# Performance work log

Measured on AMD Instinct MI355X. Metric: run time of the kernel, lower is better.

Reference implementation:

```python
import jax, jax.numpy as jnp
import numpy as np
from jax.ops import segment_sum

N_NODES = 100000
N_EDGES = 1600000
N_GRAPHS = 128


def setup_inputs() -> dict:
    key = jax.random.key(0)
    ks = jax.random.split(key, 16)
    x = jax.random.normal(ks[0], (N_NODES, 128), dtype=jnp.float32)
    edge_index = jax.random.randint(ks[1], (2, N_EDGES), 0, N_NODES, dtype=jnp.int64)
    batch = jnp.sort(jax.random.randint(ks[2], (N_NODES,), 0, N_GRAPHS, dtype=jnp.int64))
    def glorot(k, fan_in, fan_out):
        lim = (6.0 / (fan_in + fan_out)) ** 0.5
        return jax.random.uniform(k, (fan_in, fan_out), jnp.float32, -lim, lim)
    return {
        "x": x, "edge_index": edge_index, "batch": batch,
        "W1": glorot(ks[3], 128, 64), "b1": jnp.zeros((64,), jnp.float32),
        "W2": glorot(ks[4], 64, 64),  "b2": jnp.zeros((64,), jnp.float32),
        "W3": glorot(ks[5], 64, 64),  "b3": jnp.zeros((64,), jnp.float32),
        "W4": glorot(ks[6], 64, 64),  "b4": jnp.zeros((64,), jnp.float32),
        "Wl": glorot(ks[7], 64, 1),   "bl": jnp.zeros((1,), jnp.float32),
    }


def _gcn_layer(x, row, col, norm, W, b):
    # x: [N, Cin] -> [N, Cout]; gather source feats, scale, scatter-add at target
    h = x @ W                                 # dense transform first (GCNConv order)
    msg = norm[:, None] * h[row]              # [E, Cout]
    out = segment_sum(msg, col, num_segments=N_NODES)
    return out + b


def reference(x, edge_index, batch, W1, b1, W2, b2, W3, b3, W4, b4, Wl, bl):
    row, col = edge_index[0], edge_index[1]
    # symmetric degree normalization based on in-degree of col (PyG degree(col))
    deg = segment_sum(jnp.ones((N_EDGES,), x.dtype), col, num_segments=N_NODES)
    dinv = jnp.where(deg > 0, deg ** -0.5, jnp.zeros_like(deg))
    norm = dinv[row] * dinv[col]              # [E]

    h = _gcn_layer(x, row, col, norm, W1, b1)
    h = _gcn_layer(h, row, col, norm, W2, b2)
    h = _gcn_layer(h, row, col, norm, W3, b3)
    h = _gcn_layer(h, row, col, norm, W4, b4)  # [N, 64]

    # to_dense_batch + mean(dim=1): padded zeros count, so divide by max graph size
    sums = segment_sum(h, batch, num_segments=N_GRAPHS)          # [B, 64]
    counts = segment_sum(jnp.ones((N_NODES,), h.dtype), batch, num_segments=N_GRAPHS)
    n_max = jnp.max(counts)
    pooled = sums / n_max                                        # [B, 64]
    return pooled @ Wl + bl                                      # [B, 1]
```

## Files before the change

kernel.cpp:

```cpp
#include <hip/hip_runtime.h>
#include <hip/hip_bf16.h>
#include <hip/hip_fp16.h>

#define N_NODES 100000
#define N_EDGES 1600000
#define N_GRAPHS 128

#define BSH 9
#define BNODES 512
#define NB 196
#define CAP 12288
#define BLK 512
#define EPB (N_EDGES / BLK)
#define RECMAX 10240

#define SPLIT 4

typedef __attribute__((ext_vector_type(8))) _Float16 v8h;
typedef __attribute__((ext_vector_type(4))) float v4f;


__global__ __launch_bounds__(256) void k_hist(const int* __restrict__ col,
                                              int* __restrict__ hist_t) {
    __shared__ int h[NB];
    const int t = threadIdx.x, b = blockIdx.x;
    for (int i = t; i < NB; i += 256) h[i] = 0;
    __syncthreads();
    const int e0 = b * EPB;
    for (int i = t; i < EPB; i += 256) atomicAdd(&h[col[e0 + i] >> BSH], 1);
    __syncthreads();
    for (int i = t; i < NB; i += 256) hist_t[i * BLK + b] = h[i];
}

__global__ __launch_bounds__(512) void k_cursors(const int* __restrict__ hist_t,
                                                 int* __restrict__ cursors,
                                                 int* __restrict__ bcnt) {
    __shared__ int s[BLK];
    const int t = threadIdx.x, bin = blockIdx.x;
    const int v = hist_t[bin * BLK + t];
    s[t] = v; __syncthreads();
    for (int off = 1; off < BLK; off <<= 1) {
        int a = (t >= off) ? s[t - off] : 0;
        __syncthreads(); s[t] += a; __syncthreads();
    }
    cursors[bin * BLK + t] = bin * CAP + s[t] - v;
    if (t == BLK - 1) bcnt[bin] = s[t];
}

__global__ __launch_bounds__(256) void k_mid(const int* __restrict__ row,
                                             const int* __restrict__ col,
                                             const int* __restrict__ cursors,
                                             int* __restrict__ bedges) {
    __shared__ int cur[NB];
    const int t = threadIdx.x, b = blockIdx.x;
    for (int i = t; i < NB; i += 256) cur[i] = cursors[i * BLK + b];
    __syncthreads();
    const int e0 = b * EPB;
    for (int i = t; i < EPB; i += 256) {
        const int c = col[e0 + i];
        const int r = row[e0 + i];
        const int pos = atomicAdd(&cur[c >> BSH], 1);
        bedges[pos] = r | ((c & (BNODES - 1)) << 17);
    }
}

__global__ __launch_bounds__(512) void k_build(const int* __restrict__ bedges,
                                               const int* __restrict__ bcnt,
                                               int* __restrict__ csr,
                                               int* __restrict__ offs,
                                               int* __restrict__ deg_c,
                                               float* __restrict__ dinv) {
    __shared__ int rec[RECMAX];
    __shared__ int deg[BNODES];
    __shared__ int offx[BNODES];
    __shared__ int cur[BNODES];
    const int t = threadIdx.x, bin = blockIdx.x;
    const int base = bin * CAP;
    const int cnt = bcnt[bin];
    const int vb = bin << BSH;
    const int nn = min(BNODES, N_NODES - vb);
    for (int i = t; i < cnt; i += 512) rec[i] = bedges[base + i];
    deg[t] = 0;
    __syncthreads();
    for (int i = t; i < cnt; i += 512) atomicAdd(&deg[(rec[i] >> 17) & (BNODES - 1)], 1);
    __syncthreads();
    const int d = (t < nn) ? deg[t] : 0;
    const int pd = (d + 7) & ~7;
    offx[t] = pd; __syncthreads();
    for (int off = 1; off < BNODES; off <<= 1) {
        int a = (t >= off) ? offx[t - off] : 0;
        __syncthreads(); offx[t] += a; __syncthreads();
    }
    const int myoff = offx[t] - pd;
    cur[t] = myoff;
    if (t < nn) {
        offs[vb + t] = base + myoff;
        deg_c[vb + t] = d;
        dinv[vb + t] = (d > 0) ? rsqrtf((float)d) : 0.0f;
        for (int j = d; j < pd; j++) csr[base + myoff + j] = N_NODES;
    }
    __syncthreads();
    for (int i = t; i < cnt; i += 512) {
        const int r = rec[i];
        const int pos = atomicAdd(&cur[(r >> 17) & (BNODES - 1)], 1);
        csr[base + pos] = r & 0x1FFFF;
    }
}


template <int CIN, typename TIN>
__global__ __launch_bounds__(256) void k_gemm(const TIN* __restrict__ X,
                                              const float* __restrict__ W,
                                              const float* __restrict__ dinv,
                                              __half* __restrict__ H16) {
    constexpr int SA = 72;
    constexpr int SB = 72;
    __shared__ __align__(16) _Float16 sA[128 * SA];
    __shared__ __align__(16) _Float16 sBh[64 * SB];
    __shared__ __align__(16) _Float16 sBl[64 * SB];
    const int t = threadIdx.x;
    const int w = t >> 6, lane = t & 63;
    const int quad = lane >> 4, l16 = lane & 15;
    const int nb = blockIdx.x * 128;

    v4f acc[2][4] = {};

    for (int k0 = 0; k0 < CIN; k0 += 64) {
        if (k0) __syncthreads();
        for (int i = t; i < 64 * 16; i += 256) {
            const int k = i >> 4, c4 = (i & 15) * 4;
            const float4 wv = *reinterpret_cast<const float4*>(W + (size_t)(k0 + k) * 64 + c4);
            const float wf[4] = {wv.x, wv.y, wv.z, wv.w};
            #pragma unroll
            for (int j = 0; j < 4; j++) {
                const _Float16 hi = (_Float16)wf[j];
                sBh[(c4 + j) * SB + k] = hi;
                sBl[(c4 + j) * SB + k] = (_Float16)(wf[j] - (float)hi);
            }
        }
        if constexpr (sizeof(TIN) == 4) {
            for (int i = t; i < 128 * 16; i += 256) {
                const int node = i >> 4, k4 = (i & 15) * 4;
                const int gn = nb + node;
                float4 v = make_float4(0.f, 0.f, 0.f, 0.f);
                if (gn < N_NODES)
                    v = *reinterpret_cast<const float4*>((const float*)X + (size_t)gn * CIN + k0 + k4);
                _Float16* d = &sA[node * SA + k4];
                d[0] = (_Float16)v.x; d[1] = (_Float16)v.y;
                d[2] = (_Float16)v.z; d[3] = (_Float16)v.w;
            }
        } else {
            for (int i = t; i < 128 * 8; i += 256) {
                const int node = i >> 3, k8 = (i & 7) * 8;
                const int gn = nb + node;
                int4 v = make_int4(0, 0, 0, 0);
                if (gn < N_NODES)
                    v = *reinterpret_cast<const int4*>((const __half*)X + (size_t)gn * CIN + k0 + k8);
                *reinterpret_cast<int4*>(&sA[node * SA + k8]) = v;
            }
        }
        __syncthreads();

        #pragma unroll
        for (int kt = 0; kt < 2; kt++) {
            const int kb = kt * 32 + quad * 8;
            v8h afr[2], bh[4], bl[4];
            #pragma unroll
            for (int mt = 0; mt < 2; mt++)
                afr[mt] = *reinterpret_cast<const v8h*>(&sA[(w * 32 + mt * 16 + l16) * SA + kb]);
            #pragma unroll
            for (int nt = 0; nt < 4; nt++) {
                bh[nt] = *reinterpret_cast<const v8h*>(&sBh[(nt * 16 + l16) * SB + kb]);
                bl[nt] = *reinterpret_cast<const v8h*>(&sBl[(nt * 16 + l16) * SB + kb]);
            }
            #pragma unroll
            for (int mt = 0; mt < 2; mt++)
                #pragma unroll
                for (int nt = 0; nt < 4; nt++) {
                    acc[mt][nt] = __builtin_amdgcn_mfma_f32_16x16x32_f16(afr[mt], bh[nt], acc[mt][nt], 0, 0, 0);
                    acc[mt][nt] = __builtin_amdgcn_mfma_f32_16x16x32_f16(afr[mt], bl[nt], acc[mt][nt], 0, 0, 0);
                }
        }
    }

    #pragma unroll
    for (int mt = 0; mt < 2; mt++) {
        #pragma unroll
        for (int reg = 0; reg < 4; reg++) {
            const int node = nb + w * 32 + mt * 16 + quad * 4 + reg;
            if (node < N_NODES) {
                const float dv = dinv[node];
                #pragma unroll
                for (int nt = 0; nt < 4; nt++)
                    H16[(size_t)node * 64 + nt * 16 + l16] =
                        __float2half(acc[mt][nt][reg] * dv);
            }
        }
    }
}


template <typename TOUT>
__global__ __launch_bounds__(256) void k_prop(const __half* __restrict__ Hin,
                                              const int* __restrict__ csr,
                                              const int* __restrict__ offs,
                                              const int* __restrict__ deg_c,
                                              const float* __restrict__ dinv,
                                              const float* __restrict__ bias,
                                              TOUT* __restrict__ Hout) {
    const int wave = threadIdx.x >> 6, lane = threadIdx.x & 63;
    const int quad = lane >> 4;
    const int l = lane & 15;
    const int v = blockIdx.x * 16 + wave * 4 + quad;
    const int start = offs[v];
    const int cp = (deg_c[v] + 7) & ~7;
    const int* ep = csr + start;
    const __half* hb = Hin + l * 4;
    float a0 = 0.f, a1 = 0.f, a2 = 0.f, a3 = 0.f;
    for (int j = 0; j < cp; j += 8) {
        const int4 q0 = *reinterpret_cast<const int4*>(ep + j);
        const int4 q1 = *reinterpret_cast<const int4*>(ep + j + 4);
        const int2 r0 = *reinterpret_cast<const int2*>(hb + (size_t)q0.x * 64);
        const int2 r1 = *reinterpret_cast<const int2*>(hb + (size_t)q0.y * 64);
        const int2 r2 = *reinterpret_cast<const int2*>(hb + (size_t)q0.z * 64);
        const int2 r3 = *reinterpret_cast<const int2*>(hb + (size_t)q0.w * 64);
        const int2 r4 = *reinterpret_cast<const int2*>(hb + (size_t)q1.x * 64);
        const int2 r5 = *reinterpret_cast<const int2*>(hb + (size_t)q1.y * 64);
        const int2 r6 = *reinterpret_cast<const int2*>(hb + (size_t)q1.z * 64);
        const int2 r7 = *reinterpret_cast<const int2*>(hb + (size_t)q1.w * 64);
        #define ACC(r) { \
            const float2 u = __half22float2(*reinterpret_cast<const __half2*>(&r.x)); \
            const float2 w = __half22float2(*reinterpret_cast<const __half2*>(&r.y)); \
            a0 += u.x; a1 += u.y; a2 += w.x; a3 += w.y; }
        ACC(r0) ACC(r1) ACC(r2) ACC(r3) ACC(r4) ACC(r5) ACC(r6) ACC(r7)
        #undef ACC
    }
    const float dv = dinv[v];
    const float4 bs = *reinterpret_cast<const float4*>(bias + l * 4);
    const float o0 = dv * a0 + bs.x, o1 = dv * a1 + bs.y;
    const float o2 = dv * a2 + bs.z, o3 = dv * a3 + bs.w;
    if constexpr (sizeof(TOUT) == 2) {
        __half2 h[2];
        h[0] = __floats2half2_rn(o0, o1);
        h[1] = __floats2half2_rn(o2, o3);
        *reinterpret_cast<int2*>((__half*)Hout + (size_t)v * 64 + l * 4) =
            *reinterpret_cast<const int2*>(h);
    } else {
        float4 o; o.x = o0; o.y = o1; o.z = o2; o.w = o3;
        *reinterpret_cast<float4*>((float*)Hout + (size_t)v * 64 + l * 4) = o;
    }
}


__global__ __launch_bounds__(256) void k_pool(const float* __restrict__ H,
                                              const int* __restrict__ batch,
                                              float* __restrict__ partial) {
    const int g = blockIdx.x >> 2;
    const int s = blockIdx.x & (SPLIT - 1);
    int lo = 0, hi = N_NODES;
    while (lo < hi) { int m = (lo + hi) >> 1; if (batch[m] < g) lo = m + 1; else hi = m; }
    const int a = lo;
    lo = 0; hi = N_NODES;
    while (lo < hi) { int m = (lo + hi) >> 1; if (batch[m] < g + 1) lo = m + 1; else hi = m; }
    const int b = lo;

    const int wave = threadIdx.x >> 6, lane = threadIdx.x & 63;
    const int lane16 = s * 4 + wave;
    float ac0 = 0.f, ac1 = 0.f, ac2 = 0.f, ac3 = 0.f;
    int v = a + lane16;
    for (; v + 48 < b; v += 64) {
        ac0 += H[(size_t)v * 64 + lane];
        ac1 += H[(size_t)(v + 16) * 64 + lane];
        ac2 += H[(size_t)(v + 32) * 64 + lane];
        ac3 += H[(size_t)(v + 48) * 64 + lane];
    }
    for (; v < b; v += 16) ac0 += H[(size_t)v * 64 + lane];
    const float acc = (ac0 + ac1) + (ac2 + ac3);

    __shared__ float red[4][64];
    red[wave][lane] = acc;
    __syncthreads();
    if (wave == 0) {
        const float r = (red[0][lane] + red[1][lane]) + (red[2][lane] + red[3][lane]);
        partial[((size_t)s * N_GRAPHS + g) * 64 + lane] = r;
    }
}

__global__ void k_final(const float* __restrict__ partial, const int* __restrict__ batch,
                        const float* __restrict__ Wl, const float* __restrict__ bl,
                        float* __restrict__ out) {
    __shared__ int scnt[128];
    int t = threadIdx.x;
    int lo = 0, hi = N_NODES;
    while (lo < hi) { int mid = (lo + hi) >> 1; if (batch[mid] < t) lo = mid + 1; else hi = mid; }
    int a = lo;
    lo = 0; hi = N_NODES;
    while (lo < hi) { int mid = (lo + hi) >> 1; if (batch[mid] < t + 1) lo = mid + 1; else hi = mid; }
    scnt[t] = lo - a;
    __syncthreads();
    for (int off = 64; off > 0; off >>= 1) {
        if (t < off) scnt[t] = max(scnt[t], scnt[t + off]);
        __syncthreads();
    }
    const float nmax = (float)scnt[0];
    float s = 0.f;
    for (int c = 0; c < 64; c++) {
        float g = 0.f;
        #pragma unroll
        for (int p = 0; p < SPLIT; p++)
            g += partial[((size_t)p * N_GRAPHS + t) * 64 + c];
        s += g * Wl[c];
    }
    out[t] = s / nmax + bl[0];
}


extern "C" void kernel_launch(void* const* d_in, const int* in_sizes, int n_in,
                              void* d_out, int out_size, void* d_ws, size_t ws_size,
                              hipStream_t stream) {
    const float* x    = (const float*)d_in[0];
    const int*   ei   = (const int*)d_in[1];
    const int*   batch= (const int*)d_in[2];
    const float* W1 = (const float*)d_in[3];  const float* b1 = (const float*)d_in[4];
    const float* W2 = (const float*)d_in[5];  const float* b2 = (const float*)d_in[6];
    const float* W3 = (const float*)d_in[7];  const float* b3 = (const float*)d_in[8];
    const float* W4 = (const float*)d_in[9];  const float* b4 = (const float*)d_in[10];
    const float* Wl = (const float*)d_in[11]; const float* bl = (const float*)d_in[12];
    float* out = (float*)d_out;

    const int* row = ei;
    const int* col = ei + N_EDGES;

    char* ws = (char*)d_ws;
    size_t off = 0;
    auto alloc = [&](size_t bytes) {
        void* p = ws + off;
        off = (off + bytes + 255) & ~(size_t)255;
        return p;
    };
    int*    hist_t  = (int*)alloc((size_t)NB * BLK * 4);
    int*    cursors = (int*)alloc((size_t)NB * BLK * 4);
    int*    bcnt    = (int*)alloc(NB * 4);
    int*    bedges  = (int*)alloc((size_t)NB * CAP * 4);
    int*    csr     = bedges;
    int*    offs    = (int*)alloc(N_NODES * 4);
    int*    deg_c   = (int*)alloc(N_NODES * 4);
    float*  dinv    = (float*)alloc(N_NODES * 4);
    __half* h16     = (__half*)alloc((size_t)(N_NODES + 1) * 64 * 2);
    __half* h_c     = (__half*)alloc((size_t)N_NODES * 64 * 2);
    float*  h_b     = (float*)alloc((size_t)N_NODES * 64 * 4);
    float*  partial = (float*)alloc((size_t)SPLIT * N_GRAPHS * 64 * 4);

    hipMemsetAsync(h16 + (size_t)N_NODES * 64, 0, 64 * 2, stream);

    k_hist<<<BLK, 256, 0, stream>>>(col, hist_t);
    k_cursors<<<NB, 512, 0, stream>>>(hist_t, cursors, bcnt);
    k_mid<<<BLK, 256, 0, stream>>>(row, col, cursors, bedges);
    k_build<<<NB, 512, 0, stream>>>(bedges, bcnt, csr, offs, deg_c, dinv);

    const int GB = (N_NODES + 127) / 128;
    const int PB = N_NODES / 16;

    k_gemm<128, float><<<GB, 256, 0, stream>>>(x, W1, dinv, h16);
    k_prop<__half><<<PB, 256, 0, stream>>>(h16, csr, offs, deg_c, dinv, b1, h_c);
    k_gemm<64, __half><<<GB, 256, 0, stream>>>(h_c, W2, dinv, h16);
    k_prop<__half><<<PB, 256, 0, stream>>>(h16, csr, offs, deg_c, dinv, b2, h_c);
    k_gemm<64, __half><<<GB, 256, 0, stream>>>(h_c, W3, dinv, h16);
    k_prop<__half><<<PB, 256, 0, stream>>>(h16, csr, offs, deg_c, dinv, b3, h_c);
    k_gemm<64, __half><<<GB, 256, 0, stream>>>(h_c, W4, dinv, h16);
    k_prop<float><<<PB, 256, 0, stream>>>(h16, csr, offs, deg_c, dinv, b4, h_b);

    k_pool<<<N_GRAPHS * SPLIT, 256, 0, stream>>>(h_b, batch, partial);
    k_final<<<1, 128, 0, stream>>>(partial, batch, Wl, bl, out);
}
```

Baseline: 362.3 us.

## Slice node features into four 16-channel planes for cache-local gather propagation

Stores the 64-channel hidden features as four planes of 16 channels each. Propagation runs one grid dimension per plane, so each plane (about 3.2 MB in fp16) can stay resident in cache while the edge gathers run. Within a quad, lanes now split the edges four ways and combine partial sums with shuffles, and CSR padding grows to 16 with a larger bin capacity. GEMM loads, GEMM stores and pooling are updated to the sliced layout. The cost is reading the CSR index list four times and adding shuffle reductions.

```diff
diff --git a/kernel.cpp b/kernel.cpp
--- a/kernel.cpp
+++ b/kernel.cpp
@@ -9,15 +9,25 @@
 #define BSH 9
 #define BNODES 512
 #define NB 196
-#define CAP 12288
+#define CAP 18432
 #define BLK 512
 #define EPB (N_EDGES / BLK)
 #define RECMAX 10240
 
 #define SPLIT 4
 
+#define NSLICE 4
+#define SLS (N_NODES + 8)
+
 typedef __attribute__((ext_vector_type(8))) _Float16 v8h;
 typedef __attribute__((ext_vector_type(4))) float v4f;
+typedef __attribute__((ext_vector_type(4))) int vi4;
+typedef __attribute__((ext_vector_type(2))) int vi2;
+typedef __attribute__((ext_vector_type(4))) float vf4;
+
+__device__ __forceinline__ float2 h2f(int bits) {
+    return __half22float2(__builtin_bit_cast(__half2, bits));
+}
 
 
 __global__ __launch_bounds__(256) void k_hist(const int* __restrict__ col,
@@ -85,7 +95,7 @@
     for (int i = t; i < cnt; i += 512) atomicAdd(&deg[(rec[i] >> 17) & (BNODES - 1)], 1);
     __syncthreads();
     const int d = (t < nn) ? deg[t] : 0;
-    const int pd = (d + 7) & ~7;
+    const int pd = (d + 15) & ~15;
     offx[t] = pd; __syncthreads();
     for (int off = 1; off < BNODES; off <<= 1) {
         int a = (t >= off) ? offx[t - off] : 0;
@@ -151,12 +161,15 @@
             }
         } else {
             for (int i = t; i < 128 * 8; i += 256) {
-                const int node = i >> 3, k8 = (i & 7) * 8;
+                const int off8 = (i & 1) * 8;
+                const int node = (i >> 1) & 127;
+                const int sl = i >> 8;
                 const int gn = nb + node;
                 int4 v = make_int4(0, 0, 0, 0);
                 if (gn < N_NODES)
-                    v = *reinterpret_cast<const int4*>((const __half*)X + (size_t)gn * CIN + k0 + k8);
-                *reinterpret_cast<int4*>(&sA[node * SA + k8]) = v;
+                    v = *reinterpret_cast<const int4*>(
+                        (const __half*)X + ((size_t)sl * N_NODES + gn) * 16 + off8);
+                *reinterpret_cast<int4*>(&sA[node * SA + sl * 16 + off8]) = v;
             }
         }
         __syncthreads();
@@ -192,7 +205,7 @@
                 const float dv = dinv[node];
                 #pragma unroll
                 for (int nt = 0; nt < 4; nt++)
-                    H16[(size_t)node * 64 + nt * 16 + l16] =
+                    H16[((size_t)nt * SLS + node) * 16 + l16] =
                         __float2half(acc[mt][nt][reg] * dv);
             }
         }
@@ -210,44 +223,48 @@
                                               TOUT* __restrict__ Hout) {
     const int wave = threadIdx.x >> 6, lane = threadIdx.x & 63;
     const int quad = lane >> 4;
-    const int l = lane & 15;
+    const int es = (lane >> 2) & 3;
+    const int cg = lane & 3;
+    const int s = blockIdx.y;
     const int v = blockIdx.x * 16 + wave * 4 + quad;
     const int start = offs[v];
-    const int cp = (deg_c[v] + 7) & ~7;
-    const int* ep = csr + start;
-    const __half* hb = Hin + l * 4;
+    const int cp = (deg_c[v] + 15) & ~15;
+    const int* ep = csr + start + es * 4;
+    const __half* hb = Hin + (size_t)s * SLS * 16 + cg * 4;
     float a0 = 0.f, a1 = 0.f, a2 = 0.f, a3 = 0.f;
-    for (int j = 0; j < cp; j += 8) {
-        const int4 q0 = *reinterpret_cast<const int4*>(ep + j);
-        const int4 q1 = *reinterpret_cast<const int4*>(ep + j + 4);
-        const int2 r0 = *reinterpret_cast<const int2*>(hb + (size_t)q0.x * 64);
-        const int2 r1 = *reinterpret_cast<const int2*>(hb + (size_t)q0.y * 64);
-        const int2 r2 = *reinterpret_cast<const int2*>(hb + (size_t)q0.z * 64);
-        const int2 r3 = *reinterpret_cast<const int2*>(hb + (size_t)q0.w * 64);
-        const int2 r4 = *reinterpret_cast<const int2*>(hb + (size_t)q1.x * 64);
-        const int2 r5 = *reinterpret_cast<const int2*>(hb + (size_t)q1.y * 64);
-        const int2 r6 = *reinterpret_cast<const int2*>(hb + (size_t)q1.z * 64);
-        const int2 r7 = *reinterpret_cast<const int2*>(hb + (size_t)q1.w * 64);
+    for (int j = 0; j < cp; j += 16) {
+        const vi4 e = __builtin_nontemporal_load(reinterpret_cast<const vi4*>(ep + j));
+        const vi2 r0 = *reinterpret_cast<const vi2*>(hb + (size_t)e.x * 16);
+        const vi2 r1 = *reinterpret_cast<const vi2*>(hb + (size_t)e.y * 16);
+        const vi2 r2 = *reinterpret_cast<const vi2*>(hb + (size_t)e.z * 16);
+        const vi2 r3 = *reinterpret_cast<const vi2*>(hb + (size_t)e.w * 16);
         #define ACC(r) { \
-            const float2 u = __half22float2(*reinterpret_cast<const __half2*>(&r.x)); \
-            const float2 w = __half22float2(*reinterpret_cast<const __half2*>(&r.y)); \
+            const float2 u = h2f(r.x); \
+            const float2 w = h2f(r.y); \
             a0 += u.x; a1 += u.y; a2 += w.x; a3 += w.y; }
-        ACC(r0) ACC(r1) ACC(r2) ACC(r3) ACC(r4) ACC(r5) ACC(r6) ACC(r7)
+        ACC(r0) ACC(r1) ACC(r2) ACC(r3)
         #undef ACC
     }
-    const float dv = dinv[v];
-    const float4 bs = *reinterpret_cast<const float4*>(bias + l * 4);
-    const float o0 = dv * a0 + bs.x, o1 = dv * a1 + bs.y;
-    const float o2 = dv * a2 + bs.z, o3 = dv * a3 + bs.w;
-    if constexpr (sizeof(TOUT) == 2) {
-        __half2 h[2];
-        h[0] = __floats2half2_rn(o0, o1);
-        h[1] = __floats2half2_rn(o2, o3);
-        *reinterpret_cast<int2*>((__half*)Hout + (size_t)v * 64 + l * 4) =
-            *reinterpret_cast<const int2*>(h);
-    } else {
-        float4 o; o.x = o0; o.y = o1; o.z = o2; o.w = o3;
-        *reinterpret_cast<float4*>((float*)Hout + (size_t)v * 64 + l * 4) = o;
+    a0 += __shfl_xor(a0, 4); a1 += __shfl_xor(a1, 4);
+    a2 += __shfl_xor(a2, 4); a3 += __shfl_xor(a3, 4);
+    a0 += __shfl_xor(a0, 8); a1 += __shfl_xor(a1, 8);
+    a2 += __shfl_xor(a2, 8); a3 += __shfl_xor(a3, 8);
+    if (es == 0) {
+        const float dv = dinv[v];
+        const float4 bs = *reinterpret_cast<const float4*>(bias + s * 16 + cg * 4);
+        const float o0 = dv * a0 + bs.x, o1 = dv * a1 + bs.y;
+        const float o2 = dv * a2 + bs.z, o3 = dv * a3 + bs.w;
+        if constexpr (sizeof(TOUT) == 2) {
+            vi2 pk;
+            pk.x = __builtin_bit_cast(int, __floats2half2_rn(o0, o1));
+            pk.y = __builtin_bit_cast(int, __floats2half2_rn(o2, o3));
+            __builtin_nontemporal_store(pk,
+                reinterpret_cast<vi2*>((__half*)Hout + ((size_t)s * N_NODES + v) * 16 + cg * 4));
+        } else {
+            vf4 o; o.x = o0; o.y = o1; o.z = o2; o.w = o3;
+            __builtin_nontemporal_store(o,
+                reinterpret_cast<vf4*>((float*)Hout + ((size_t)s * N_NODES + v) * 16 + cg * 4));
+        }
     }
 }
 
@@ -266,15 +283,16 @@
 
     const int wave = threadIdx.x >> 6, lane = threadIdx.x & 63;
     const int lane16 = s * 4 + wave;
+    const size_t sbase = (size_t)(lane >> 4) * ((size_t)N_NODES * 16) + (lane & 15);
     float ac0 = 0.f, ac1 = 0.f, ac2 = 0.f, ac3 = 0.f;
     int v = a + lane16;
     for (; v + 48 < b; v += 64) {
-        ac0 += H[(size_t)v * 64 + lane];
-        ac1 += H[(size_t)(v + 16) * 64 + lane];
-        ac2 += H[(size_t)(v + 32) * 64 + lane];
-        ac3 += H[(size_t)(v + 48) * 64 + lane];
-    }
-    for (; v < b; v += 16) ac0 += H[(size_t)v * 64 + lane];
+        ac0 += H[sbase + (size_t)v * 16];
+        ac1 += H[sbase + (size_t)(v + 16) * 16];
+        ac2 += H[sbase + (size_t)(v + 32) * 16];
+        ac3 += H[sbase + (size_t)(v + 48) * 16];
+    }
+    for (; v < b; v += 16) ac0 += H[sbase + (size_t)v * 16];
     const float acc = (ac0 + ac1) + (ac2 + ac3);
 
     __shared__ float red[4][64];
@@ -346,12 +364,13 @@
     int*    offs    = (int*)alloc(N_NODES * 4);
     int*    deg_c   = (int*)alloc(N_NODES * 4);
     float*  dinv    = (float*)alloc(N_NODES * 4);
-    __half* h16     = (__half*)alloc((size_t)(N_NODES + 1) * 64 * 2);
-    __half* h_c     = (__half*)alloc((size_t)N_NODES * 64 * 2);
-    float*  h_b     = (float*)alloc((size_t)N_NODES * 64 * 4);
+    __half* h16     = (__half*)alloc((size_t)NSLICE * SLS * 16 * 2);
+    __half* h_c     = (__half*)alloc((size_t)NSLICE * N_NODES * 16 * 2);
+    float*  h_b     = (float*)alloc((size_t)NSLICE * N_NODES * 16 * 4);
     float*  partial = (float*)alloc((size_t)SPLIT * N_GRAPHS * 64 * 4);
 
-    hipMemsetAsync(h16 + (size_t)N_NODES * 64, 0, 64 * 2, stream);
+    for (int s = 0; s < NSLICE; ++s)
+        (void)hipMemsetAsync(h16 + ((size_t)s * SLS + N_NODES) * 16, 0, 16 * 2, stream);
 
     k_hist<<<BLK, 256, 0, stream>>>(col, hist_t);
     k_cursors<<<NB, 512, 0, stream>>>(hist_t, cursors, bcnt);
@@ -359,16 +378,16 @@
     k_build<<<NB, 512, 0, stream>>>(bedges, bcnt, csr, offs, deg_c, dinv);
 
     const int GB = (N_NODES + 127) / 128;
-    const int PB = N_NODES / 16;
+    const dim3 gprop(N_NODES / 16, NSLICE);
 
     k_gemm<128, float><<<GB, 256, 0, stream>>>(x, W1, dinv, h16);
-    k_prop<__half><<<PB, 256, 0, stream>>>(h16, csr, offs, deg_c, dinv, b1, h_c);
+    k_prop<__half><<<gprop, 256, 0, stream>>>(h16, csr, offs, deg_c, dinv, b1, h_c);
     k_gemm<64, __half><<<GB, 256, 0, stream>>>(h_c, W2, dinv, h16);
-    k_prop<__half><<<PB, 256, 0, stream>>>(h16, csr, offs, deg_c, dinv, b2, h_c);
+    k_prop<__half><<<gprop, 256, 0, stream>>>(h16, csr, offs, deg_c, dinv, b2, h_c);
     k_gemm<64, __half><<<GB, 256, 0, stream>>>(h_c, W3, dinv, h16);
-    k_prop<__half><<<PB, 256, 0, stream>>>(h16, csr, offs, deg_c, dinv, b3, h_c);
+    k_prop<__half><<<gprop, 256, 0, stream>>>(h16, csr, offs, deg_c, dinv, b3, h_c);
     k_gemm<64, __half><<<GB, 256, 0, stream>>>(h_c, W4, dinv, h16);
-    k_prop<float><<<PB, 256, 0, stream>>>(h16, csr, offs, deg_c, dinv, b4, h_b);
+    k_prop<float><<<gprop, 256, 0, stream>>>(h16, csr, offs, deg_c, dinv, b4, h_b);
 
     k_pool<<<N_GRAPHS * SPLIT, 256, 0, stream>>>(h_b, batch, partial);
     k_final<<<1, 128, 0, stream>>>(partial, batch, Wl, bl, out);
```

After: 503.9 us. 1.39x slower.

## Fuse propagation with next-layer GEMM and use nontemporal CSR loads

Applied to the files above, without the earlier changes.

Merges each intermediate propagation (gather-sum over CSR neighbors) with the following layer's dense transform into one kernel. The aggregated 128-node tile is written straight to LDS as fp16 and fed to MFMA, so the h_c round trip and three kernel launches go away. It also adds nontemporal loads for CSR indices and a nontemporal store for the final fp32 output. The cost is fewer blocks (782 vs 6250) doing latency-bound gathers with large LDS per block, which may lower occupancy and latency hiding.

```diff
diff --git a/kernel.cpp b/kernel.cpp
--- a/kernel.cpp
+++ b/kernel.cpp
@@ -18,6 +18,13 @@
 
 typedef __attribute__((ext_vector_type(8))) _Float16 v8h;
 typedef __attribute__((ext_vector_type(4))) float v4f;
+typedef __attribute__((ext_vector_type(4))) int vi4;
+typedef __attribute__((ext_vector_type(2))) int vi2;
+typedef __attribute__((ext_vector_type(4))) float vf4;
+
+__device__ __forceinline__ float2 h2f(int bits) {
+    return __half22float2(__builtin_bit_cast(__half2, bits));
+}
 
 
 __global__ __launch_bounds__(256) void k_hist(const int* __restrict__ col,
@@ -108,8 +115,8 @@
 }
 
 
-template <int CIN, typename TIN>
-__global__ __launch_bounds__(256) void k_gemm(const TIN* __restrict__ X,
+template <int CIN>
+__global__ __launch_bounds__(256) void k_gemm(const float* __restrict__ X,
                                               const float* __restrict__ W,
                                               const float* __restrict__ dinv,
                                               __half* __restrict__ H16) {
@@ -138,26 +145,15 @@
                 sBl[(c4 + j) * SB + k] = (_Float16)(wf[j] - (float)hi);
             }
         }
-        if constexpr (sizeof(TIN) == 4) {
-            for (int i = t; i < 128 * 16; i += 256) {
-                const int node = i >> 4, k4 = (i & 15) * 4;
-                const int gn = nb + node;
-                float4 v = make_float4(0.f, 0.f, 0.f, 0.f);
-                if (gn < N_NODES)
-                    v = *reinterpret_cast<const float4*>((const float*)X + (size_t)gn * CIN + k0 + k4);
-                _Float16* d = &sA[node * SA + k4];
-                d[0] = (_Float16)v.x; d[1] = (_Float16)v.y;
-                d[2] = (_Float16)v.z; d[3] = (_Float16)v.w;
-            }
-        } else {
-            for (int i = t; i < 128 * 8; i += 256) {
-                const int node = i >> 3, k8 = (i & 7) * 8;
-                const int gn = nb + node;
-                int4 v = make_int4(0, 0, 0, 0);
-                if (gn < N_NODES)
-                    v = *reinterpret_cast<const int4*>((const __half*)X + (size_t)gn * CIN + k0 + k8);
-                *reinterpret_cast<int4*>(&sA[node * SA + k8]) = v;
-            }
+        for (int i = t; i < 128 * 16; i += 256) {
+            const int node = i >> 4, k4 = (i & 15) * 4;
+            const int gn = nb + node;
+            float4 v = make_float4(0.f, 0.f, 0.f, 0.f);
+            if (gn < N_NODES)
+                v = *reinterpret_cast<const float4*>(X + (size_t)gn * CIN + k0 + k4);
+            _Float16* d = &sA[node * SA + k4];
+            d[0] = (_Float16)v.x; d[1] = (_Float16)v.y;
+            d[2] = (_Float16)v.z; d[3] = (_Float16)v.w;
         }
         __syncthreads();
 
@@ -200,14 +196,13 @@
 }
 
 
-template <typename TOUT>
-__global__ __launch_bounds__(256) void k_prop(const __half* __restrict__ Hin,
-                                              const int* __restrict__ csr,
-                                              const int* __restrict__ offs,
-                                              const int* __restrict__ deg_c,
-                                              const float* __restrict__ dinv,
-                                              const float* __restrict__ bias,
-                                              TOUT* __restrict__ Hout) {
+__global__ __launch_bounds__(256) void k_prop_f(const __half* __restrict__ Hin,
+                                                const int* __restrict__ csr,
+                                                const int* __restrict__ offs,
+                                                const int* __restrict__ deg_c,
+                                                const float* __restrict__ dinv,
+                                                const float* __restrict__ bias,
+                                                float* __restrict__ Hout) {
     const int wave = threadIdx.x >> 6, lane = threadIdx.x & 63;
     const int quad = lane >> 4;
     const int l = lane & 15;
@@ -218,36 +213,136 @@
     const __half* hb = Hin + l * 4;
     float a0 = 0.f, a1 = 0.f, a2 = 0.f, a3 = 0.f;
     for (int j = 0; j < cp; j += 8) {
-        const int4 q0 = *reinterpret_cast<const int4*>(ep + j);
-        const int4 q1 = *reinterpret_cast<const int4*>(ep + j + 4);
-        const int2 r0 = *reinterpret_cast<const int2*>(hb + (size_t)q0.x * 64);
-        const int2 r1 = *reinterpret_cast<const int2*>(hb + (size_t)q0.y * 64);
-        const int2 r2 = *reinterpret_cast<const int2*>(hb + (size_t)q0.z * 64);
-        const int2 r3 = *reinterpret_cast<const int2*>(hb + (size_t)q0.w * 64);
-        const int2 r4 = *reinterpret_cast<const int2*>(hb + (size_t)q1.x * 64);
-        const int2 r5 = *reinterpret_cast<const int2*>(hb + (size_t)q1.y * 64);
-        const int2 r6 = *reinterpret_cast<const int2*>(hb + (size_t)q1.z * 64);
-        const int2 r7 = *reinterpret_cast<const int2*>(hb + (size_t)q1.w * 64);
+        const vi4 q0 = __builtin_nontemporal_load(reinterpret_cast<const vi4*>(ep + j));
+        const vi4 q1 = __builtin_nontemporal_load(reinterpret_cast<const vi4*>(ep + j + 4));
+        const vi2 r0 = *reinterpret_cast<const vi2*>(hb + (size_t)q0.x * 64);
+        const vi2 r1 = *reinterpret_cast<const vi2*>(hb + (size_t)q0.y * 64);
+        const vi2 r2 = *reinterpret_cast<const vi2*>(hb + (size_t)q0.z * 64);
+        const vi2 r3 = *reinterpret_cast<const vi2*>(hb + (size_t)q0.w * 64);
+        const vi2 r4 = *reinterpret_cast<const vi2*>(hb + (size_t)q1.x * 64);
+        const vi2 r5 = *reinterpret_cast<const vi2*>(hb + (size_t)q1.y * 64);
+        const vi2 r6 = *reinterpret_cast<const vi2*>(hb + (size_t)q1.z * 64);
+        const vi2 r7 = *reinterpret_cast<const vi2*>(hb + (size_t)q1.w * 64);
         #define ACC(r) { \
-            const float2 u = __half22float2(*reinterpret_cast<const __half2*>(&r.x)); \
-            const float2 w = __half22float2(*reinterpret_cast<const __half2*>(&r.y)); \
-            a0 += u.x; a1 += u.y; a2 += w.x; a3 += w.y; }
+            const float2 u = h2f(r.x); \
+            const float2 w2 = h2f(r.y); \
+            a0 += u.x; a1 += u.y; a2 += w2.x; a3 += w2.y; }
         ACC(r0) ACC(r1) ACC(r2) ACC(r3) ACC(r4) ACC(r5) ACC(r6) ACC(r7)
         #undef ACC
     }
     const float dv = dinv[v];
     const float4 bs = *reinterpret_cast<const float4*>(bias + l * 4);
-    const float o0 = dv * a0 + bs.x, o1 = dv * a1 + bs.y;
-    const float o2 = dv * a2 + bs.z, o3 = dv * a3 + bs.w;
-    if constexpr (sizeof(TOUT) == 2) {
-        __half2 h[2];
-        h[0] = __floats2half2_rn(o0, o1);
-        h[1] = __floats2half2_rn(o2, o3);
-        *reinterpret_cast<int2*>((__half*)Hout + (size_t)v * 64 + l * 4) =
-            *reinterpret_cast<const int2*>(h);
-    } else {
-        float4 o; o.x = o0; o.y = o1; o.z = o2; o.w = o3;
-        *reinterpret_cast<float4*>((float*)Hout + (size_t)v * 64 + l * 4) = o;
+    vf4 o;
+    o.x = dv * a0 + bs.x; o.y = dv * a1 + bs.y;
+    o.z = dv * a2 + bs.z; o.w = dv * a3 + bs.w;
+    __builtin_nontemporal_store(o,
+        reinterpret_cast<vf4*>(Hout + (size_t)v * 64 + l * 4));
+}
+
+
+__global__ __launch_bounds__(256) void k_fused(const __half* __restrict__ Hin,
+                                               const int* __restrict__ csr,
+                                               const int* __restrict__ offs,
+                                               const int* __restrict__ deg_c,
+                                               const float* __restrict__ dinv,
+                                               const float* __restrict__ biasp,
+                                               const float* __restrict__ W,
+                                               __half* __restrict__ H16) {
+    constexpr int SA = 72;
+    constexpr int SB = 72;
+    __shared__ __align__(16) _Float16 sA[128 * SA];
+    __shared__ __align__(16) _Float16 sBh[64 * SB];
+    __shared__ __align__(16) _Float16 sBl[64 * SB];
+    const int t = threadIdx.x;
+    const int w = t >> 6, lane = t & 63;
+    const int quad = lane >> 4, l16 = lane & 15;
+    const int nb = blockIdx.x * 128;
+
+    for (int i = t; i < 64 * 16; i += 256) {
+        const int k = i >> 4, c4 = (i & 15) * 4;
+        const float4 wv = *reinterpret_cast<const float4*>(W + (size_t)k * 64 + c4);
+        const float wf[4] = {wv.x, wv.y, wv.z, wv.w};
+        #pragma unroll
+        for (int j = 0; j < 4; j++) {
+            const _Float16 hi = (_Float16)wf[j];
+            sBh[(c4 + j) * SB + k] = hi;
+            sBl[(c4 + j) * SB + k] = (_Float16)(wf[j] - (float)hi);
+        }
+    }
+
+    const float4 bs = *reinterpret_cast<const float4*>(biasp + l16 * 4);
+    const __half* hb = Hin + l16 * 4;
+    for (int r = 0; r < 8; r++) {
+        const int ln = r * 16 + w * 4 + quad;
+        const int v = nb + ln;
+        float a0 = 0.f, a1 = 0.f, a2 = 0.f, a3 = 0.f;
+        if (v < N_NODES) {
+            const int start = offs[v];
+            const int cp = (deg_c[v] + 7) & ~7;
+            const int* ep = csr + start;
+            for (int j = 0; j < cp; j += 8) {
+                const vi4 q0 = __builtin_nontemporal_load(reinterpret_cast<const vi4*>(ep + j));
+                const vi4 q1 = __builtin_nontemporal_load(reinterpret_cast<const vi4*>(ep + j + 4));
+                const vi2 r0 = *reinterpret_cast<const vi2*>(hb + (size_t)q0.x * 64);
+                const vi2 r1 = *reinterpret_cast<const vi2*>(hb + (size_t)q0.y * 64);
+                const vi2 r2 = *reinterpret_cast<const vi2*>(hb + (size_t)q0.z * 64);
+                const vi2 r3 = *reinterpret_cast<const vi2*>(hb + (size_t)q0.w * 64);
+                const vi2 r4 = *reinterpret_cast<const vi2*>(hb + (size_t)q1.x * 64);
+                const vi2 r5 = *reinterpret_cast<const vi2*>(hb + (size_t)q1.y * 64);
+                const vi2 r6 = *reinterpret_cast<const vi2*>(hb + (size_t)q1.z * 64);
+                const vi2 r7 = *reinterpret_cast<const vi2*>(hb + (size_t)q1.w * 64);
+                #define ACC(rr) { \
+                    const float2 u = h2f(rr.x); \
+                    const float2 w2 = h2f(rr.y); \
+                    a0 += u.x; a1 += u.y; a2 += w2.x; a3 += w2.y; }
+                ACC(r0) ACC(r1) ACC(r2) ACC(r3) ACC(r4) ACC(r5) ACC(r6) ACC(r7)
+                #undef ACC
+            }
+            const float dv = dinv[v];
+            a0 = dv * a0 + bs.x; a1 = dv * a1 + bs.y;
+            a2 = dv * a2 + bs.z; a3 = dv * a3 + bs.w;
+        }
+        vi2 pk;
+        pk.x = __builtin_bit_cast(int, __floats2half2_rn(a0, a1));
+        pk.y = __builtin_bit_cast(int, __floats2half2_rn(a2, a3));
+        *reinterpret_cast<vi2*>(&sA[ln * SA + l16 * 4]) = pk;
+    }
+    __syncthreads();
+
+    v4f acc[2][4] = {};
+    #pragma unroll
+    for (int kt = 0; kt < 2; kt++) {
+        const int kb = kt * 32 + quad * 8;
+        v8h afr[2], bh[4], bl[4];
+        #pragma unroll
+        for (int mt = 0; mt < 2; mt++)
+            afr[mt] = *reinterpret_cast<const v8h*>(&sA[(w * 32 + mt * 16 + l16) * SA + kb]);
+        #pragma unroll
+        for (int nt = 0; nt < 4; nt++) {
+            bh[nt] = *reinterpret_cast<const v8h*>(&sBh[(nt * 16 + l16) * SB + kb]);
+            bl[nt] = *reinterpret_cast<const v8h*>(&sBl[(nt * 16 + l16) * SB + kb]);
+        }
+        #pragma unroll
+        for (int mt = 0; mt < 2; mt++)
+            #pragma unroll
+            for (int nt = 0; nt < 4; nt++) {
+                acc[mt][nt] = __builtin_amdgcn_mfma_f32_16x16x32_f16(afr[mt], bh[nt], acc[mt][nt], 0, 0, 0);
+                acc[mt][nt] = __builtin_amdgcn_mfma_f32_16x16x32_f16(afr[mt], bl[nt], acc[mt][nt], 0, 0, 0);
+            }
+    }
+    #pragma unroll
+    for (int mt = 0; mt < 2; mt++) {
+        #pragma unroll
+        for (int reg = 0; reg < 4; reg++) {
+            const int node = nb + w * 32 + mt * 16 + quad * 4 + reg;
+            if (node < N_NODES) {
+                const float dv = dinv[node];
+                #pragma unroll
+                for (int nt = 0; nt < 4; nt++)
+                    H16[(size_t)node * 64 + nt * 16 + l16] =
+                        __float2half(acc[mt][nt][reg] * dv);
+            }
+        }
     }
 }
 
@@ -346,12 +441,13 @@
     int*    offs    = (int*)alloc(N_NODES * 4);
     int*    deg_c   = (int*)alloc(N_NODES * 4);
     float*  dinv    = (float*)alloc(N_NODES * 4);
-    __half* h16     = (__half*)alloc((size_t)(N_NODES + 1) * 64 * 2);
-    __half* h_c     = (__half*)alloc((size_t)N_NODES * 64 * 2);
+    __half* h16a    = (__half*)alloc((size_t)(N_NODES + 1) * 64 * 2);
+    __half* h16b    = (__half*)alloc((size_t)(N_NODES + 1) * 64 * 2);
     float*  h_b     = (float*)alloc((size_t)N_NODES * 64 * 4);
     float*  partial = (float*)alloc((size_t)SPLIT * N_GRAPHS * 64 * 4);
 
-    hipMemsetAsync(h16 + (size_t)N_NODES * 64, 0, 64 * 2, stream);
+    (void)hipMemsetAsync(h16a + (size_t)N_NODES * 64, 0, 64 * 2, stream);
+    (void)hipMemsetAsync(h16b + (size_t)N_NODES * 64, 0, 64 * 2, stream);
 
     k_hist<<<BLK, 256, 0, stream>>>(col, hist_t);
     k_cursors<<<NB, 512, 0, stream>>>(hist_t, cursors, bcnt);
@@ -361,14 +457,11 @@
     const int GB = (N_NODES + 127) / 128;
     const int PB = N_NODES / 16;
 
-    k_gemm<128, float><<<GB, 256, 0, stream>>>(x, W1, dinv, h16);
-    k_prop<__half><<<PB, 256, 0, stream>>>(h16, csr, offs, deg_c, dinv, b1, h_c);
-    k_gemm<64, __half><<<GB, 256, 0, stream>>>(h_c, W2, dinv, h16);
-    k_prop<__half><<<PB, 256, 0, stream>>>(h16, csr, offs, deg_c, dinv, b2, h_c);
-    k_gemm<64, __half><<<GB, 256, 0, stream>>>(h_c, W3, dinv, h16);
-    k_prop<__half><<<PB, 256, 0, stream>>>(h16, csr, offs, deg_c, dinv, b3, h_c);
-    k_gemm<64, __half><<<GB, 256, 0, stream>>>(h_c, W4, dinv, h16);
-    k_prop<float><<<PB, 256, 0, stream>>>(h16, csr, offs, deg_c, dinv, b4, h_b);
+    k_gemm<128><<<GB, 256, 0, stream>>>(x, W1, dinv, h16a);
+    k_fused<<<GB, 256, 0, stream>>>(h16a, csr, offs, deg_c, dinv, b1, W2, h16b);
+    k_fused<<<GB, 256, 0, stream>>>(h16b, csr, offs, deg_c, dinv, b2, W3, h16a);
+    k_fused<<<GB, 256, 0, stream>>>(h16a, csr, offs, deg_c, dinv, b3, W4, h16b);
+    k_prop_f<<<PB, 256, 0, stream>>>(h16b, csr, offs, deg_c, dinv, b4, h_b);
 
     k_pool<<<N_GRAPHS * SPLIT, 256, 0, stream>>>(h_b, batch, partial);
     k_final<<<1, 128, 0, stream>>>(partial, batch, Wl, bl, out);
```

Result: slower. 393.7 us (+8.7%).

## Load GEMM A fragments directly from global and add nontemporal hints in propagation

Applied to the files above, without the earlier changes.

The dense transform kernel now stages the whole weight matrix (hi/lo fp16 split) in shared memory once, and each wave loads its A-operand fragments straight from global memory into registers. This drops the shared-memory A tile and the per-k-chunk barriers. Blocks shrink to 64 nodes, which doubles the grid. The propagation kernel marks CSR index loads and the final fp32 output stores as nontemporal, to reduce cache pollution from streamed data and keep gathered feature rows resident. The trade-off is that direct-from-global A loads are less coalesced and more weight conversion work is repeated across twice as many blocks.

```diff
diff --git a/kernel.cpp b/kernel.cpp
--- a/kernel.cpp
+++ b/kernel.cpp
@@ -18,6 +18,19 @@
 
 typedef __attribute__((ext_vector_type(8))) _Float16 v8h;
 typedef __attribute__((ext_vector_type(4))) float v4f;
+typedef __attribute__((ext_vector_type(4))) int vi4;
+typedef __attribute__((ext_vector_type(2))) int vi2;
+typedef __attribute__((ext_vector_type(4))) float vf4;
+
+__device__ __forceinline__ float2 h2f(int bits) {
+    return __half22float2(__builtin_bit_cast(__half2, bits));
+}
+
+__device__ __forceinline__ v8h zero8h() {
+    v8h z = {(_Float16)0, (_Float16)0, (_Float16)0, (_Float16)0,
+             (_Float16)0, (_Float16)0, (_Float16)0, (_Float16)0};
+    return z;
+}
 
 
 __global__ __launch_bounds__(256) void k_hist(const int* __restrict__ col,
@@ -113,88 +126,70 @@
                                               const float* __restrict__ W,
                                               const float* __restrict__ dinv,
                                               __half* __restrict__ H16) {
-    constexpr int SA = 72;
-    constexpr int SB = 72;
-    __shared__ __align__(16) _Float16 sA[128 * SA];
-    __shared__ __align__(16) _Float16 sBh[64 * SB];
-    __shared__ __align__(16) _Float16 sBl[64 * SB];
+    constexpr int SBK = CIN + 8;
+    __shared__ __align__(16) _Float16 sBh[64 * SBK];
+    __shared__ __align__(16) _Float16 sBl[64 * SBK];
     const int t = threadIdx.x;
     const int w = t >> 6, lane = t & 63;
     const int quad = lane >> 4, l16 = lane & 15;
-    const int nb = blockIdx.x * 128;
-
-    v4f acc[2][4] = {};
-
-    for (int k0 = 0; k0 < CIN; k0 += 64) {
-        if (k0) __syncthreads();
-        for (int i = t; i < 64 * 16; i += 256) {
-            const int k = i >> 4, c4 = (i & 15) * 4;
-            const float4 wv = *reinterpret_cast<const float4*>(W + (size_t)(k0 + k) * 64 + c4);
-            const float wf[4] = {wv.x, wv.y, wv.z, wv.w};
-            #pragma unroll
-            for (int j = 0; j < 4; j++) {
-                const _Float16 hi = (_Float16)wf[j];
-                sBh[(c4 + j) * SB + k] = hi;
-                sBl[(c4 + j) * SB + k] = (_Float16)(wf[j] - (float)hi);
-            }
-        }
-        if constexpr (sizeof(TIN) == 4) {
-            for (int i = t; i < 128 * 16; i += 256) {
-                const int node = i >> 4, k4 = (i & 15) * 4;
-                const int gn = nb + node;
-                float4 v = make_float4(0.f, 0.f, 0.f, 0.f);
-                if (gn < N_NODES)
-                    v = *reinterpret_cast<const float4*>((const float*)X + (size_t)gn * CIN + k0 + k4);
-                _Float16* d = &sA[node * SA + k4];
-                d[0] = (_Float16)v.x; d[1] = (_Float16)v.y;
-                d[2] = (_Float16)v.z; d[3] = (_Float16)v.w;
+    const int nb = blockIdx.x * 64;
+
+    for (int i = t; i < CIN * 16; i += 256) {
+        const int k = i >> 4, c4 = (i & 15) * 4;
+        const float4 wv = *reinterpret_cast<const float4*>(W + (size_t)k * 64 + c4);
+        const float wf[4] = {wv.x, wv.y, wv.z, wv.w};
+        #pragma unroll
+        for (int j = 0; j < 4; j++) {
+            const _Float16 hi = (_Float16)wf[j];
+            sBh[(c4 + j) * SBK + k] = hi;
+            sBl[(c4 + j) * SBK + k] = (_Float16)(wf[j] - (float)hi);
+        }
+    }
+    __syncthreads();
+
+    const int gn = nb + w * 16 + l16;
+    v4f acc[4] = {};
+
+    #pragma unroll
+    for (int k0 = 0; k0 < CIN; k0 += 32) {
+        const int kb = k0 + quad * 8;
+        v8h afr;
+        if (gn < N_NODES) {
+            if constexpr (sizeof(TIN) == 2) {
+                afr = *reinterpret_cast<const v8h*>((const __half*)X + (size_t)gn * CIN + kb);
+            } else {
+                const float4 u0 = *reinterpret_cast<const float4*>((const float*)X + (size_t)gn * CIN + kb);
+                const float4 u1 = *reinterpret_cast<const float4*>((const float*)X + (size_t)gn * CIN + kb + 4);
+                afr[0] = (_Float16)u0.x; afr[1] = (_Float16)u0.y;
+                afr[2] = (_Float16)u0.z; afr[3] = (_Float16)u0.w;
+                afr[4] = (_Float16)u1.x; afr[5] = (_Float16)u1.y;
+                afr[6] = (_Float16)u1.z; afr[7] = (_Float16)u1.w;
             }
         } else {
-            for (int i = t; i < 128 * 8; i += 256) {
-                const int node = i >> 3, k8 = (i & 7) * 8;
-                const int gn = nb + node;
-                int4 v = make_int4(0, 0, 0, 0);
-                if (gn < N_NODES)
-                    v = *reinterpret_cast<const int4*>((const __half*)X + (size_t)gn * CIN + k0 + k8);
-                *reinterpret_cast<int4*>(&sA[node * SA + k8]) = v;
-            }
-        }
-        __syncthreads();
-
+            afr = zero8h();
+        }
+        v8h bh[4], bl[4];
         #pragma unroll
-        for (int kt = 0; kt < 2; kt++) {
-            const int kb = kt * 32 + quad * 8;
-            v8h afr[2], bh[4], bl[4];
+        for (int nt = 0; nt < 4; nt++) {
+            bh[nt] = *reinterpret_cast<const v8h*>(&sBh[(nt * 16 + l16) * SBK + kb]);
+            bl[nt] = *reinterpret_cast<const v8h*>(&sBl[(nt * 16 + l16) * SBK + kb]);
+        }
+        #pragma unroll
+        for (int nt = 0; nt < 4; nt++) {
+            acc[nt] = __builtin_amdgcn_mfma_f32_16x16x32_f16(afr, bh[nt], acc[nt], 0, 0, 0);
+            acc[nt] = __builtin_amdgcn_mfma_f32_16x16x32_f16(afr, bl[nt], acc[nt], 0, 0, 0);
+        }
+    }
+
+    #pragma unroll
+    for (int reg = 0; reg < 4; reg++) {
+        const int node = nb + w * 16 + quad * 4 + reg;
+        if (node < N_NODES) {
+            const float dv = dinv[node];
             #pragma unroll
-            for (int mt = 0; mt < 2; mt++)
-                afr[mt] = *reinterpret_cast<const v8h*>(&sA[(w * 32 + mt * 16 + l16) * SA + kb]);
-            #pragma unroll
-            for (int nt = 0; nt < 4; nt++) {
-                bh[nt] = *reinterpret_cast<const v8h*>(&sBh[(nt * 16 + l16) * SB + kb]);
-                bl[nt] = *reinterpret_cast<const v8h*>(&sBl[(nt * 16 + l16) * SB + kb]);
-            }
-            #pragma unroll
-            for (int mt = 0; mt < 2; mt++)
-                #pragma unroll
-                for (int nt = 0; nt < 4; nt++) {
-                    acc[mt][nt] = __builtin_amdgcn_mfma_f32_16x16x32_f16(afr[mt], bh[nt], acc[mt][nt], 0, 0, 0);
-                    acc[mt][nt] = __builtin_amdgcn_mfma_f32_16x16x32_f16(afr[mt], bl[nt], acc[mt][nt], 0, 0, 0);
-                }
-        }
-    }
-
-    #pragma unroll
-    for (int mt = 0; mt < 2; mt++) {
-        #pragma unroll
-        for (int reg = 0; reg < 4; reg++) {
-            const int node = nb + w * 32 + mt * 16 + quad * 4 + reg;
-            if (node < N_NODES) {
-                const float dv = dinv[node];
-                #pragma unroll
-                for (int nt = 0; nt < 4; nt++)
-                    H16[(size_t)node * 64 + nt * 16 + l16] =
-                        __float2half(acc[mt][nt][reg] * dv);
-            }
+            for (int nt = 0; nt < 4; nt++)
+                H16[(size_t)node * 64 + nt * 16 + l16] =
+                    __float2half(acc[nt][reg] * dv);
         }
     }
 }
@@ -218,20 +213,20 @@
     const __half* hb = Hin + l * 4;
     float a0 = 0.f, a1 = 0.f, a2 = 0.f, a3 = 0.f;
     for (int j = 0; j < cp; j += 8) {
-        const int4 q0 = *reinterpret_cast<const int4*>(ep + j);
-        const int4 q1 = *reinterpret_cast<const int4*>(ep + j + 4);
-        const int2 r0 = *reinterpret_cast<const int2*>(hb + (size_t)q0.x * 64);
-        const int2 r1 = *reinterpret_cast<const int2*>(hb + (size_t)q0.y * 64);
-        const int2 r2 = *reinterpret_cast<const int2*>(hb + (size_t)q0.z * 64);
-        const int2 r3 = *reinterpret_cast<const int2*>(hb + (size_t)q0.w * 64);
-        const int2 r4 = *reinterpret_cast<const int2*>(hb + (size_t)q1.x * 64);
-        const int2 r5 = *reinterpret_cast<const int2*>(hb + (size_t)q1.y * 64);
-        const int2 r6 = *reinterpret_cast<const int2*>(hb + (size_t)q1.z * 64);
-        const int2 r7 = *reinterpret_cast<const int2*>(hb + (size_t)q1.w * 64);
+        const vi4 q0 = __builtin_nontemporal_load(reinterpret_cast<const vi4*>(ep + j));
+        const vi4 q1 = __builtin_nontemporal_load(reinterpret_cast<const vi4*>(ep + j + 4));
+        const vi2 r0 = *reinterpret_cast<const vi2*>(hb + (size_t)q0.x * 64);
+        const vi2 r1 = *reinterpret_cast<const vi2*>(hb + (size_t)q0.y * 64);
+        const vi2 r2 = *reinterpret_cast<const vi2*>(hb + (size_t)q0.z * 64);
+        const vi2 r3 = *reinterpret_cast<const vi2*>(hb + (size_t)q0.w * 64);
+        const vi2 r4 = *reinterpret_cast<const vi2*>(hb + (size_t)q1.x * 64);
+        const vi2 r5 = *reinterpret_cast<const vi2*>(hb + (size_t)q1.y * 64);
+        const vi2 r6 = *reinterpret_cast<const vi2*>(hb + (size_t)q1.z * 64);
+        const vi2 r7 = *reinterpret_cast<const vi2*>(hb + (size_t)q1.w * 64);
         #define ACC(r) { \
-            const float2 u = __half22float2(*reinterpret_cast<const __half2*>(&r.x)); \
-            const float2 w = __half22float2(*reinterpret_cast<const __half2*>(&r.y)); \
-            a0 += u.x; a1 += u.y; a2 += w.x; a3 += w.y; }
+            const float2 u = h2f(r.x); \
+            const float2 w2 = h2f(r.y); \
+            a0 += u.x; a1 += u.y; a2 += w2.x; a3 += w2.y; }
         ACC(r0) ACC(r1) ACC(r2) ACC(r3) ACC(r4) ACC(r5) ACC(r6) ACC(r7)
         #undef ACC
     }
@@ -240,14 +235,14 @@
     const float o0 = dv * a0 + bs.x, o1 = dv * a1 + bs.y;
     const float o2 = dv * a2 + bs.z, o3 = dv * a3 + bs.w;
     if constexpr (sizeof(TOUT) == 2) {
-        __half2 h[2];
-        h[0] = __floats2half2_rn(o0, o1);
-        h[1] = __floats2half2_rn(o2, o3);
-        *reinterpret_cast<int2*>((__half*)Hout + (size_t)v * 64 + l * 4) =
-            *reinterpret_cast<const int2*>(h);
+        vi2 pk;
+        pk.x = __builtin_bit_cast(int, __floats2half2_rn(o0, o1));
+        pk.y = __builtin_bit_cast(int, __floats2half2_rn(o2, o3));
+        *reinterpret_cast<vi2*>((__half*)Hout + (size_t)v * 64 + l * 4) = pk;
     } else {
-        float4 o; o.x = o0; o.y = o1; o.z = o2; o.w = o3;
-        *reinterpret_cast<float4*>((float*)Hout + (size_t)v * 64 + l * 4) = o;
+        vf4 o; o.x = o0; o.y = o1; o.z = o2; o.w = o3;
+        __builtin_nontemporal_store(o,
+            reinterpret_cast<vf4*>((float*)Hout + (size_t)v * 64 + l * 4));
     }
 }
 
@@ -351,14 +346,14 @@
     float*  h_b     = (float*)alloc((size_t)N_NODES * 64 * 4);
     float*  partial = (float*)alloc((size_t)SPLIT * N_GRAPHS * 64 * 4);
 
-    hipMemsetAsync(h16 + (size_t)N_NODES * 64, 0, 64 * 2, stream);
+    (void)hipMemsetAsync(h16 + (size_t)N_NODES * 64, 0, 64 * 2, stream);
 
     k_hist<<<BLK, 256, 0, stream>>>(col, hist_t);
     k_cursors<<<NB, 512, 0, stream>>>(hist_t, cursors, bcnt);
     k_mid<<<BLK, 256, 0, stream>>>(row, col, cursors, bedges);
     k_build<<<NB, 512, 0, stream>>>(bedges, bcnt, csr, offs, deg_c, dinv);
 
-    const int GB = (N_NODES + 127) / 128;
+    const int GB = (N_NODES + 63) / 64;
     const int PB = N_NODES / 16;
 
     k_gemm<128, float><<<GB, 256, 0, stream>>>(x, W1, dinv, h16);
```

Measured after the change: 378.2 us. +4.4%, slower.
